# Kernel tuning notes

Measured on AMD Instinct MI355X. Metric: run time of the kernel, lower is better.

The kernel has to match this reference:

```python
import jax, jax.numpy as jnp
import numpy as np

D_MODEL = 1024
NUM_HEADS = 16
D_HEAD = D_MODEL // NUM_HEADS
B, T_Q, T_K = 2, 2048, 2048


def setup_inputs() -> dict:
    key = jax.random.key(0)
    ks = jax.random.split(key, 7)
    s = 0.02
    return {
        "query": jax.random.normal(ks[0], (B, T_Q, D_MODEL), jnp.float32),
        "key_value": jax.random.normal(ks[1], (B, T_K, D_MODEL), jnp.float32),
        "mask": jax.random.randint(ks[2], (B, 1, T_Q, T_K), 0, 2, jnp.int32),
        "rel_pos_bias": jax.random.normal(ks[3], (NUM_HEADS, T_Q, T_K), jnp.float32),
        "Wq": jax.random.normal(ks[4], (D_MODEL, D_MODEL), jnp.float32) * s,
        "Wkv": jax.random.normal(ks[5], (D_MODEL, 2 * D_MODEL), jnp.float32) * s,
        "Wo": jax.random.normal(ks[6], (D_MODEL, D_MODEL), jnp.float32) * s,
    }


def reference(query, key_value, mask, rel_pos_bias, Wq, Wkv, Wo):
    Bq, Tq, D = query.shape
    Tk = key_value.shape[1]
    H, Dh = NUM_HEADS, D_HEAD
    q = (query @ Wq).reshape(Bq, Tq, H, Dh)              # [B,Tq,H,Dh]
    kv = (key_value @ Wkv).reshape(Bq, Tk, 2, H, Dh)
    k, v = kv[:, :, 0], kv[:, :, 1]                      # [B,Tk,H,Dh]
    scale = 1.0 / jnp.sqrt(jnp.asarray(Dh, q.dtype))
    scores = jnp.einsum("bqhd,bkhd->bhqk", q, k) * scale  # [B,H,Tq,Tk]
    scores = scores + rel_pos_bias[None]                  # bias broadcast over batch
    scores = jnp.where(mask == 0, -jnp.inf, scores)
    attn = jax.nn.softmax(scores, axis=-1)
    out = jnp.einsum("bhqk,bkhd->bqhd", attn, v).reshape(Bq, Tq, D)
    return out @ Wo
```

## Files before the change

### kernel.cpp

```cpp
#include <hip/hip_runtime.h>

typedef unsigned short u16;
typedef unsigned int u32;
typedef unsigned long long u64;
typedef __attribute__((ext_vector_type(4))) float f32x4;
typedef __attribute__((ext_vector_type(4))) unsigned short u16x4;
typedef __attribute__((ext_vector_type(8))) short short8;

#define GLOAD16(G, L) __builtin_amdgcn_global_load_lds( \
    (const __attribute__((address_space(1))) void*)(G), \
    (__attribute__((address_space(3))) void*)(L), 16, 0, 0)

__device__ __forceinline__ u16 f2bf(float f) {
  union { float f; unsigned u; } c; c.f = f;
  unsigned u = c.u;
  u += 0x7FFFu + ((u >> 16) & 1u);
  return (u16)(u >> 16);
}

__device__ __forceinline__ void store_out(u16* p, float v) { *p = f2bf(v); }
__device__ __forceinline__ void store_out(float* p, float v) { *p = v; }

__global__ void k_cvt(const float* __restrict__ in, u16* __restrict__ out, int n4) {
  int i = blockIdx.x * blockDim.x + threadIdx.x;
  if (i >= n4) return;
  const f32x4 v = *(const f32x4*)(in + (size_t)i * 4);
  u16x4 o;
  o[0] = f2bf(v[0]); o[1] = f2bf(v[1]); o[2] = f2bf(v[2]); o[3] = f2bf(v[3]);
  *(u16x4*)(out + (size_t)i * 4) = o;
}

__global__ void k_tcvt(const float* __restrict__ src, u16* __restrict__ dst,
                       int R, int C, float scale) {
  __shared__ float t[32][33];
  int bx = blockIdx.x * 32;
  int by = blockIdx.y * 32;
  int tx = threadIdx.x, ty = threadIdx.y;
  #pragma unroll
  for (int j = 0; j < 32; j += 8)
    t[ty + j][tx] = src[(size_t)(by + ty + j) * C + bx + tx];
  __syncthreads();
  #pragma unroll
  for (int j = 0; j < 32; j += 8)
    dst[(size_t)(bx + ty + j) * R + by + tx] = f2bf(t[tx][ty + j] * scale);
}

__global__ void k_tv(const u16* __restrict__ kv, u16* __restrict__ vt) {
  __shared__ u16 sh[32][34];
  int b = blockIdx.z;
  int tb = blockIdx.x * 32;
  int db = blockIdx.y * 32;
  int tx = threadIdx.x, ty = threadIdx.y;
  #pragma unroll
  for (int j = 0; j < 32; j += 8)
    sh[ty + j][tx] = kv[(size_t)(b * 2048 + tb + ty + j) * 2048 + 1024 + db + tx];
  __syncthreads();
  int t = tb + tx;
  int k6 = t & 63;
  int colp = (t & ~63) | (((k6 >> 2) & 3) << 4) | ((k6 >> 4) << 2) | (k6 & 3);
  #pragma unroll
  for (int j = 0; j < 32; j += 8)
    vt[(size_t)(b * 1024 + db + ty + j) * 2048 + colp] = sh[tx][ty + j];
}

__global__ void k_pm(const int* __restrict__ mask, unsigned* __restrict__ bits, int nw) {
  int w = blockIdx.x * blockDim.x + threadIdx.x;
  if (w >= nw) return;
  const int4* p = (const int4*)(mask + (size_t)w * 32);
  unsigned b = 0;
  #pragma unroll
  for (int j = 0; j < 8; ++j) {
    int4 v = p[j];
    b |= (v.x != 0 ? 1u : 0u) << (j * 4);
    b |= (v.y != 0 ? 1u : 0u) << (j * 4 + 1);
    b |= (v.z != 0 ? 1u : 0u) << (j * 4 + 2);
    b |= (v.w != 0 ? 1u : 0u) << (j * 4 + 3);
  }
  bits[w] = b;
}

template <int BM, int BN, typename OUT_T>
__global__ __launch_bounds__(256) void k_gemm(
    const u16* __restrict__ A, const u16* __restrict__ Bt,
    OUT_T* __restrict__ C, int M, int N, int K)
{
  constexpr int MI = BM / 32, NI = BN / 32;
  __shared__ u16 As[BM * 64];
  __shared__ u16 Bs[BN * 64];
  const int tid = threadIdx.x;
  const int lane = tid & 63;
  const int w = tid >> 6;
  const int wr = w >> 1, wc = w & 1;
  const int l16 = lane & 15, lh = lane >> 4;
  const size_t tm = blockIdx.x, tn = blockIdx.y;

  f32x4 acc[MI][NI] = {};

  for (int kt = 0; kt < K; kt += 64) {
    #pragma unroll
    for (int i = 0; i < BM / 32; ++i) {
      int flat = i * 256 + tid;
      int row = flat >> 3, cb = flat & 7;
      GLOAD16(A + (tm * BM + row) * K + kt + ((cb ^ (row & 7)) * 8),
              (char*)As + flat * 16);
    }
    #pragma unroll
    for (int i = 0; i < BN / 32; ++i) {
      int flat = i * 256 + tid;
      int row = flat >> 3, cb = flat & 7;
      GLOAD16(Bt + (tn * BN + row) * K + kt + ((cb ^ (row & 7)) * 8),
              (char*)Bs + flat * 16);
    }
    __syncthreads();
    #pragma unroll
    for (int kk = 0; kk < 2; ++kk) {
      short8 a[MI], b[NI];
      #pragma unroll
      for (int mi = 0; mi < MI; ++mi) {
        int row = wr * (BM / 2) + mi * 16 + l16;
        a[mi] = *(const short8*)&As[row * 64 + ((kk * 32 + lh * 8) ^ ((row & 7) * 8))];
      }
      #pragma unroll
      for (int ni = 0; ni < NI; ++ni) {
        int row = wc * (BN / 2) + ni * 16 + l16;
        b[ni] = *(const short8*)&Bs[row * 64 + ((kk * 32 + lh * 8) ^ ((row & 7) * 8))];
      }
      #pragma unroll
      for (int mi = 0; mi < MI; ++mi)
        #pragma unroll
        for (int ni = 0; ni < NI; ++ni)
          acc[mi][ni] = __builtin_amdgcn_mfma_f32_16x16x32_bf16(a[mi], b[ni], acc[mi][ni], 0, 0, 0);
    }
    __syncthreads();
  }
  #pragma unroll
  for (int mi = 0; mi < MI; ++mi)
    #pragma unroll
    for (int ni = 0; ni < NI; ++ni)
      #pragma unroll
      for (int r = 0; r < 4; ++r) {
        size_t row = tm * BM + wr * (BM / 2) + mi * 16 + lh * 4 + r;
        size_t col = tn * BN + wc * (BN / 2) + ni * 16 + l16;
        store_out(&C[row * N + col], acc[mi][ni][r]);
      }
}

__global__ __launch_bounds__(512, 4) void k_attn(
    const u16* __restrict__ Qp,
    const u16* __restrict__ KVp,
    const u16* __restrict__ Vt,
    const float* __restrict__ bias,
    const unsigned* __restrict__ mbits,
    u16* __restrict__ Ob)
{
  __shared__ u16 Ks[2 * 2 * 64 * 64];
  __shared__ u16 Vs[2 * 2 * 64 * 64];
  const int tid = threadIdx.x;
  const int lane = tid & 63;
  const int w = tid >> 6;
  const int bw = w >> 2;
  const int qs = (w & 3) * 16;
  const int qt = blockIdx.x;
  const int h  = blockIdx.y;
  const int l16 = lane & 15, lh = lane >> 4;
  const int q = qt * 64 + qs + l16;

  const int srow = tid >> 3, scb = tid & 7;
  const u16* ksrc = KVp + (size_t)srow * 2048 + h * 64 + ((scb ^ (srow & 7)) * 8);
  const u16* vsrc = Vt + ((size_t)(h * 64 + srow)) * 2048 + ((scb ^ (srow & 7)) * 8);

  short8 qf[2];
  {
    size_t row = (size_t)bw * 2048 + q;
    qf[0] = *(const short8*)&Qp[row * 1024 + h * 64 + lh * 8];
    qf[1] = *(const short8*)&Qp[row * 1024 + h * 64 + 32 + lh * 8];
  }

  const float* bsrc = bias + ((size_t)h * 2048 + q) * 2048 + lh * 4;
  const u64*   msrc = (const u64*)(mbits + ((size_t)bw * 2048 + q) * 64);

  f32x4 oacc[4] = {};
  f32x4 lpv = {};
  f32x4 biasA[4], biasB[4];
  u64 mwA, mwB;

  GLOAD16(ksrc,                       &Ks[tid * 8]);
  GLOAD16(ksrc + (size_t)2048 * 2048, &Ks[4096 + tid * 8]);
  GLOAD16(vsrc,                       &Vs[tid * 8]);
  GLOAD16(vsrc + (size_t)1024 * 2048, &Vs[4096 + tid * 8]);
  biasA[0] = *(const f32x4*)(bsrc +  0);
  biasA[1] = *(const f32x4*)(bsrc + 16);
  biasA[2] = *(const f32x4*)(bsrc + 32);
  biasA[3] = *(const f32x4*)(bsrc + 48);
  mwA = msrc[0];
  asm volatile("s_waitcnt vmcnt(0)" ::: "memory");
  __builtin_amdgcn_s_barrier();

#define ASTEP(KT, CUR, BC, MC, BN_, MN_) do {                                            \
    const int ktn_ = ((KT) + 1 < 32) ? (KT) + 1 : 31;                                    \
    GLOAD16(ksrc + (size_t)ktn_ * 64 * 2048,                  &Ks[((CUR)^1) * 8192 + tid * 8]);        \
    GLOAD16(ksrc + ((size_t)2048 + (size_t)ktn_ * 64) * 2048, &Ks[((CUR)^1) * 8192 + 4096 + tid * 8]); \
    GLOAD16(vsrc + (size_t)ktn_ * 64,                         &Vs[((CUR)^1) * 8192 + tid * 8]);        \
    GLOAD16(vsrc + (size_t)1024 * 2048 + (size_t)ktn_ * 64,   &Vs[((CUR)^1) * 8192 + 4096 + tid * 8]); \
    __builtin_amdgcn_sched_barrier(0);                                                   \
    f32x4 s_[4];                                                                         \
    s_[0] = BC[0]; s_[1] = BC[1]; s_[2] = BC[2]; s_[3] = BC[3];                          \
    const unsigned tlo_ = (unsigned)(MC) >> (lh * 4);                                    \
    const unsigned thi_ = (unsigned)((MC) >> 32) >> (lh * 4);                            \
    BN_[0] = *(const f32x4*)(bsrc + (size_t)ktn_ * 64 +  0);                             \
    BN_[1] = *(const f32x4*)(bsrc + (size_t)ktn_ * 64 + 16);                             \
    BN_[2] = *(const f32x4*)(bsrc + (size_t)ktn_ * 64 + 32);                             \
    BN_[3] = *(const f32x4*)(bsrc + (size_t)ktn_ * 64 + 48);                             \
    MN_ = msrc[ktn_];                                                                    \
    const int kb_ = (CUR) * 8192 + bw * 4096;                                            \
    _Pragma("unroll")                                                                    \
    for (int kk = 0; kk < 2; ++kk) {                                                     \
      short8 kf_[4];                                                                     \
      _Pragma("unroll")                                                                  \
      for (int ni = 0; ni < 4; ++ni) {                                                   \
        const int row_ = ni * 16 + l16;                                                  \
        kf_[ni] = *(const short8*)&Ks[kb_ + row_ * 64 + ((kk * 32 + lh * 8) ^ ((row_ & 7) * 8))]; \
      }                                                                                  \
      _Pragma("unroll")                                                                  \
      for (int ni = 0; ni < 4; ++ni)                                                     \
        s_[ni] = __builtin_amdgcn_mfma_f32_16x16x32_bf16(kf_[ni], qf[kk], s_[ni], 0, 0, 0); \
    }                                                                                    \
    _Pragma("unroll")                                                                    \
    for (int kk = 0; kk < 2; ++kk) {                                                     \
      union { u32 wd[4]; short8 v; } pf_;                                                \
      _Pragma("unroll")                                                                  \
      for (int half = 0; half < 2; ++half) {                                             \
        const int ni = 2 * kk + half;                                                    \
        const unsigned tw_ = (ni < 2) ? tlo_ : thi_;                                     \
        _Pragma("unroll")                                                                \
        for (int r = 0; r < 4; ++r) {                                                    \
          const unsigned bit_ = (tw_ >> ((ni & 1) * 16 + r)) & 1u;                       \
          float pv_ = bit_ ? __expf(s_[ni][r]) : 0.f;                                    \
          s_[ni][r] = pv_;                                                               \
        }                                                                                \
        lpv += s_[ni];                                                                   \
        asm("v_cvt_pk_bf16_f32 %0, %1, %2" : "=v"(pf_.wd[2*half])   : "v"(s_[ni][0]), "v"(s_[ni][1])); \
        asm("v_cvt_pk_bf16_f32 %0, %1, %2" : "=v"(pf_.wd[2*half+1]) : "v"(s_[ni][2]), "v"(s_[ni][3])); \
      }                                                                                  \
      _Pragma("unroll")                                                                  \
      for (int di = 0; di < 4; ++di) {                                                   \
        const int row_ = di * 16 + l16;                                                  \
        short8 vf_ = *(const short8*)&Vs[kb_ + row_ * 64 + (((lh * 2 + kk) * 8) ^ ((row_ & 7) * 8))]; \
        oacc[di] = __builtin_amdgcn_mfma_f32_16x16x32_bf16(vf_, pf_.v, oacc[di], 0, 0, 0); \
      }                                                                                  \
    }                                                                                    \
    asm volatile("s_waitcnt lgkmcnt(0)" ::: "memory");                                   \
    asm volatile("s_waitcnt vmcnt(5)" ::: "memory");                                     \
    __builtin_amdgcn_s_barrier();                                                        \
  } while (0)

  for (int kt2 = 0; kt2 < 32; kt2 += 2) {
    ASTEP(kt2,     0, biasA, mwA, biasB, mwB);
    ASTEP(kt2 + 1, 1, biasB, mwB, biasA, mwA);
  }
#undef ASTEP

  float lpart = lpv[0] + lpv[1] + lpv[2] + lpv[3];
  lpart += __shfl_xor(lpart, 16);
  lpart += __shfl_xor(lpart, 32);
  float inv = 1.0f / lpart;
  size_t orow = (size_t)bw * 2048 + q;
  #pragma unroll
  for (int di = 0; di < 4; ++di)
    #pragma unroll
    for (int rp = 0; rp < 2; ++rp) {
      float v0 = oacc[di][2 * rp] * inv;
      float v1 = oacc[di][2 * rp + 1] * inv;
      u32 pk;
      asm("v_cvt_pk_bf16_f32 %0, %1, %2" : "=v"(pk) : "v"(v0), "v"(v1));
      *(u32*)&Ob[orow * 1024 + h * 64 + di * 16 + lh * 4 + rp * 2] = pk;
    }
}

extern "C" void kernel_launch(void* const* d_in, const int* in_sizes, int n_in,
                              void* d_out, int out_size, void* d_ws, size_t ws_size,
                              hipStream_t stream) {
  const float* query     = (const float*)d_in[0];
  const float* key_value = (const float*)d_in[1];
  const int*   mask      = (const int*)d_in[2];
  const float* bias      = (const float*)d_in[3];
  const float* Wq        = (const float*)d_in[4];
  const float* Wkv       = (const float*)d_in[5];
  const float* Wo        = (const float*)d_in[6];
  float* out = (float*)d_out;

  char* ws = (char*)d_ws;
  u16* qb   = (u16*)(ws);
  u16* kvb  = (u16*)(ws + 8388608);
  u16* WqT  = (u16*)(ws + 16777216);
  u16* WkvT = (u16*)(ws + 18874368);
  u16* WoT  = (u16*)(ws + 23068672);
  u16* Qp   = (u16*)(ws + 25165824);
  u16* KVp  = (u16*)(ws + 33554432);
  u16* Vt   = (u16*)(ws + 50331648);
  u16* Ob   = (u16*)(ws + 58720256);
  unsigned* mb = (unsigned*)(ws + 67108864);

  dim3 tb(32, 8);
  k_cvt<<<4096, 256, 0, stream>>>(query, qb, 1048576);
  k_cvt<<<4096, 256, 0, stream>>>(key_value, kvb, 1048576);
  k_tcvt<<<dim3(32, 32), tb, 0, stream>>>(Wq,  WqT,  1024, 1024, 0.125f);
  k_tcvt<<<dim3(64, 32), tb, 0, stream>>>(Wkv, WkvT, 1024, 2048, 1.0f);
  k_tcvt<<<dim3(32, 32), tb, 0, stream>>>(Wo,  WoT,  1024, 1024, 1.0f);
  k_pm<<<1024, 256, 0, stream>>>(mask, mb, 262144);
  k_gemm<64, 128, u16><<<dim3(64, 8),  256, 0, stream>>>(qb,  WqT,  Qp,  4096, 1024, 1024);
  k_gemm<64, 128, u16><<<dim3(64, 16), 256, 0, stream>>>(kvb, WkvT, KVp, 4096, 2048, 1024);
  k_tv<<<dim3(64, 32, 2), tb, 0, stream>>>(KVp, Vt);
  k_attn<<<dim3(32, 16), 512, 0, stream>>>(Qp, KVp, Vt, bias, mb, Ob);
  k_gemm<64, 128, float><<<dim3(64, 8), 256, 0, stream>>>(Ob, WoT, out, 4096, 1024, 1024);
}
```

Measured before the change: 223.1 us.

## Process two query sub-tiles per wave in attention to reuse K/V fragments

The attention block drops from 512 to 256 threads, and each wave now handles 32 query rows (two 16-row sub-tiles) instead of 16. Each K and V fragment read from LDS therefore feeds two MFMAs, halving LDS reads per unit of compute, and each thread issues twice as many global-to-LDS copies. s_setprio is raised around the MFMA sections to favour matrix issue. The cost is roughly double the accumulator and bias registers per thread plus fewer waves per block, which may reduce occupancy and latency hiding for the bias and mask loads.

```diff
diff --git a/kernel.cpp b/kernel.cpp
--- a/kernel.cpp
+++ b/kernel.cpp
@@ -145,7 +145,7 @@
       }
 }
 
-__global__ __launch_bounds__(512, 4) void k_attn(
+__global__ __launch_bounds__(256, 2) void k_attn(
     const u16* __restrict__ Qp,
     const u16* __restrict__ KVp,
     const u16* __restrict__ Vt,
@@ -158,61 +158,87 @@
   const int tid = threadIdx.x;
   const int lane = tid & 63;
   const int w = tid >> 6;
-  const int bw = w >> 2;
-  const int qs = (w & 3) * 16;
+  const int bw = w >> 1;
+  const int qs = (w & 1) * 32;
   const int qt = blockIdx.x;
   const int h  = blockIdx.y;
   const int l16 = lane & 15, lh = lane >> 4;
-  const int q = qt * 64 + qs + l16;
-
-  const int srow = tid >> 3, scb = tid & 7;
-  const u16* ksrc = KVp + (size_t)srow * 2048 + h * 64 + ((scb ^ (srow & 7)) * 8);
-  const u16* vsrc = Vt + ((size_t)(h * 64 + srow)) * 2048 + ((scb ^ (srow & 7)) * 8);
-
-  short8 qf[2];
+  const int q0 = qt * 64 + qs + l16;
+
+  const int sr0 = tid >> 3;
+  const int sc0 = (((tid & 7)) ^ (sr0 & 7)) * 8;
+  const int sr1 = (256 + tid) >> 3;
+  const int sc1 = ((((256 + tid) & 7)) ^ (sr1 & 7)) * 8;
+  const u16* k0 = KVp + (size_t)sr0 * 2048 + h * 64 + sc0;
+  const u16* k1 = KVp + (size_t)sr1 * 2048 + h * 64 + sc1;
+  const u16* v0 = Vt + (size_t)(h * 64 + sr0) * 2048 + sc0;
+  const u16* v1 = Vt + (size_t)(h * 64 + sr1) * 2048 + sc1;
+
+  short8 qf0[2], qf1[2];
   {
-    size_t row = (size_t)bw * 2048 + q;
-    qf[0] = *(const short8*)&Qp[row * 1024 + h * 64 + lh * 8];
-    qf[1] = *(const short8*)&Qp[row * 1024 + h * 64 + 32 + lh * 8];
-  }
-
-  const float* bsrc = bias + ((size_t)h * 2048 + q) * 2048 + lh * 4;
-  const u64*   msrc = (const u64*)(mbits + ((size_t)bw * 2048 + q) * 64);
-
-  f32x4 oacc[4] = {};
-  f32x4 lpv = {};
-  f32x4 biasA[4], biasB[4];
-  u64 mwA, mwB;
-
-  GLOAD16(ksrc,                       &Ks[tid * 8]);
-  GLOAD16(ksrc + (size_t)2048 * 2048, &Ks[4096 + tid * 8]);
-  GLOAD16(vsrc,                       &Vs[tid * 8]);
-  GLOAD16(vsrc + (size_t)1024 * 2048, &Vs[4096 + tid * 8]);
-  biasA[0] = *(const f32x4*)(bsrc +  0);
-  biasA[1] = *(const f32x4*)(bsrc + 16);
-  biasA[2] = *(const f32x4*)(bsrc + 32);
-  biasA[3] = *(const f32x4*)(bsrc + 48);
-  mwA = msrc[0];
+    size_t row = (size_t)bw * 2048 + q0;
+    qf0[0] = *(const short8*)&Qp[row * 1024 + h * 64 + lh * 8];
+    qf0[1] = *(const short8*)&Qp[row * 1024 + h * 64 + 32 + lh * 8];
+    qf1[0] = *(const short8*)&Qp[(row + 16) * 1024 + h * 64 + lh * 8];
+    qf1[1] = *(const short8*)&Qp[(row + 16) * 1024 + h * 64 + 32 + lh * 8];
+  }
+
+  const float* bsrc0 = bias + ((size_t)h * 2048 + q0) * 2048 + lh * 4;
+  const float* bsrc1 = bsrc0 + (size_t)16 * 2048;
+  const u64* msrc0 = (const u64*)(mbits + ((size_t)bw * 2048 + q0) * 64);
+  const u64* msrc1 = msrc0 + 16 * 32;
+
+  f32x4 oacc0[4] = {}, oacc1[4] = {};
+  f32x4 lpv0 = {}, lpv1 = {};
+  f32x4 bA0[4], bA1[4], bB0[4], bB1[4];
+  u64 mA0, mA1, mB0, mB1;
+
+  GLOAD16(k0,                       &Ks[tid * 8]);
+  GLOAD16(k1,                       &Ks[2048 + tid * 8]);
+  GLOAD16(k0 + (size_t)2048 * 2048, &Ks[4096 + tid * 8]);
+  GLOAD16(k1 + (size_t)2048 * 2048, &Ks[6144 + tid * 8]);
+  GLOAD16(v0,                       &Vs[tid * 8]);
+  GLOAD16(v1,                       &Vs[2048 + tid * 8]);
+  GLOAD16(v0 + (size_t)1024 * 2048, &Vs[4096 + tid * 8]);
+  GLOAD16(v1 + (size_t)1024 * 2048, &Vs[6144 + tid * 8]);
+  #pragma unroll
+  for (int ni = 0; ni < 4; ++ni) {
+    bA0[ni] = *(const f32x4*)(bsrc0 + ni * 16);
+    bA1[ni] = *(const f32x4*)(bsrc1 + ni * 16);
+  }
+  mA0 = msrc0[0];
+  mA1 = msrc1[0];
   asm volatile("s_waitcnt vmcnt(0)" ::: "memory");
   __builtin_amdgcn_s_barrier();
 
-#define ASTEP(KT, CUR, BC, MC, BN_, MN_) do {                                            \
+#define ASTEP(KT, CUR, BC0, BC1, MC0, MC1, BN0, BN1, MN0, MN1) do {                      \
     const int ktn_ = ((KT) + 1 < 32) ? (KT) + 1 : 31;                                    \
-    GLOAD16(ksrc + (size_t)ktn_ * 64 * 2048,                  &Ks[((CUR)^1) * 8192 + tid * 8]);        \
-    GLOAD16(ksrc + ((size_t)2048 + (size_t)ktn_ * 64) * 2048, &Ks[((CUR)^1) * 8192 + 4096 + tid * 8]); \
-    GLOAD16(vsrc + (size_t)ktn_ * 64,                         &Vs[((CUR)^1) * 8192 + tid * 8]);        \
-    GLOAD16(vsrc + (size_t)1024 * 2048 + (size_t)ktn_ * 64,   &Vs[((CUR)^1) * 8192 + 4096 + tid * 8]); \
+    const int nb_ = (CUR) ^ 1;                                                           \
+    GLOAD16(k0 + (size_t)ktn_ * 64 * 2048,                  &Ks[nb_ * 8192 + tid * 8]);  \
+    GLOAD16(k1 + (size_t)ktn_ * 64 * 2048,                  &Ks[nb_ * 8192 + 2048 + tid * 8]); \
+    GLOAD16(k0 + ((size_t)2048 + ktn_ * 64) * 2048,         &Ks[nb_ * 8192 + 4096 + tid * 8]); \
+    GLOAD16(k1 + ((size_t)2048 + ktn_ * 64) * 2048,         &Ks[nb_ * 8192 + 6144 + tid * 8]); \
+    GLOAD16(v0 + (size_t)ktn_ * 64,                         &Vs[nb_ * 8192 + tid * 8]);  \
+    GLOAD16(v1 + (size_t)ktn_ * 64,                         &Vs[nb_ * 8192 + 2048 + tid * 8]); \
+    GLOAD16(v0 + (size_t)1024 * 2048 + ktn_ * 64,           &Vs[nb_ * 8192 + 4096 + tid * 8]); \
+    GLOAD16(v1 + (size_t)1024 * 2048 + ktn_ * 64,           &Vs[nb_ * 8192 + 6144 + tid * 8]); \
     __builtin_amdgcn_sched_barrier(0);                                                   \
-    f32x4 s_[4];                                                                         \
-    s_[0] = BC[0]; s_[1] = BC[1]; s_[2] = BC[2]; s_[3] = BC[3];                          \
-    const unsigned tlo_ = (unsigned)(MC) >> (lh * 4);                                    \
-    const unsigned thi_ = (unsigned)((MC) >> 32) >> (lh * 4);                            \
-    BN_[0] = *(const f32x4*)(bsrc + (size_t)ktn_ * 64 +  0);                             \
-    BN_[1] = *(const f32x4*)(bsrc + (size_t)ktn_ * 64 + 16);                             \
-    BN_[2] = *(const f32x4*)(bsrc + (size_t)ktn_ * 64 + 32);                             \
-    BN_[3] = *(const f32x4*)(bsrc + (size_t)ktn_ * 64 + 48);                             \
-    MN_ = msrc[ktn_];                                                                    \
+    f32x4 s0_[4], s1_[4];                                                                \
+    _Pragma("unroll")                                                                    \
+    for (int ni = 0; ni < 4; ++ni) { s0_[ni] = BC0[ni]; s1_[ni] = BC1[ni]; }             \
+    const unsigned tlo0_ = (unsigned)(MC0) >> (lh * 4);                                  \
+    const unsigned thi0_ = (unsigned)((MC0) >> 32) >> (lh * 4);                          \
+    const unsigned tlo1_ = (unsigned)(MC1) >> (lh * 4);                                  \
+    const unsigned thi1_ = (unsigned)((MC1) >> 32) >> (lh * 4);                          \
+    _Pragma("unroll")                                                                    \
+    for (int ni = 0; ni < 4; ++ni) {                                                     \
+      BN0[ni] = *(const f32x4*)(bsrc0 + (size_t)ktn_ * 64 + ni * 16);                    \
+      BN1[ni] = *(const f32x4*)(bsrc1 + (size_t)ktn_ * 64 + ni * 16);                    \
+    }                                                                                    \
+    MN0 = msrc0[ktn_];                                                                   \
+    MN1 = msrc1[ktn_];                                                                   \
     const int kb_ = (CUR) * 8192 + bw * 4096;                                            \
+    __builtin_amdgcn_s_setprio(1);                                                       \
     _Pragma("unroll")                                                                    \
     for (int kk = 0; kk < 2; ++kk) {                                                     \
       short8 kf_[4];                                                                     \
@@ -222,59 +248,89 @@
         kf_[ni] = *(const short8*)&Ks[kb_ + row_ * 64 + ((kk * 32 + lh * 8) ^ ((row_ & 7) * 8))]; \
       }                                                                                  \
       _Pragma("unroll")                                                                  \
-      for (int ni = 0; ni < 4; ++ni)                                                     \
-        s_[ni] = __builtin_amdgcn_mfma_f32_16x16x32_bf16(kf_[ni], qf[kk], s_[ni], 0, 0, 0); \
+      for (int ni = 0; ni < 4; ++ni) {                                                   \
+        s0_[ni] = __builtin_amdgcn_mfma_f32_16x16x32_bf16(kf_[ni], qf0[kk], s0_[ni], 0, 0, 0); \
+        s1_[ni] = __builtin_amdgcn_mfma_f32_16x16x32_bf16(kf_[ni], qf1[kk], s1_[ni], 0, 0, 0); \
+      }                                                                                  \
     }                                                                                    \
+    __builtin_amdgcn_s_setprio(0);                                                       \
+    union pfu_ { u32 wd[4]; short8 v; };                                                 \
+    union pfu_ pf0_[2], pf1_[2];                                                         \
+    _Pragma("unroll")                                                                    \
+    for (int ni = 0; ni < 4; ++ni) {                                                     \
+      const unsigned tw0_ = (ni < 2) ? tlo0_ : thi0_;                                    \
+      const unsigned tw1_ = (ni < 2) ? tlo1_ : thi1_;                                    \
+      _Pragma("unroll")                                                                  \
+      for (int r = 0; r < 4; ++r) {                                                      \
+        const unsigned b0_ = (tw0_ >> ((ni & 1) * 16 + r)) & 1u;                         \
+        const unsigned b1_ = (tw1_ >> ((ni & 1) * 16 + r)) & 1u;                         \
+        s0_[ni][r] = b0_ ? __expf(s0_[ni][r]) : 0.f;                                     \
+        s1_[ni][r] = b1_ ? __expf(s1_[ni][r]) : 0.f;                                     \
+      }                                                                                  \
+      lpv0 += s0_[ni];                                                                   \
+      lpv1 += s1_[ni];                                                                   \
+      asm("v_cvt_pk_bf16_f32 %0, %1, %2" : "=v"(pf0_[ni >> 1].wd[2 * (ni & 1)])     : "v"(s0_[ni][0]), "v"(s0_[ni][1])); \
+      asm("v_cvt_pk_bf16_f32 %0, %1, %2" : "=v"(pf0_[ni >> 1].wd[2 * (ni & 1) + 1]) : "v"(s0_[ni][2]), "v"(s0_[ni][3])); \
+      asm("v_cvt_pk_bf16_f32 %0, %1, %2" : "=v"(pf1_[ni >> 1].wd[2 * (ni & 1)])     : "v"(s1_[ni][0]), "v"(s1_[ni][1])); \
+      asm("v_cvt_pk_bf16_f32 %0, %1, %2" : "=v"(pf1_[ni >> 1].wd[2 * (ni & 1) + 1]) : "v"(s1_[ni][2]), "v"(s1_[ni][3])); \
+    }                                                                                    \
+    __builtin_amdgcn_s_setprio(1);                                                       \
     _Pragma("unroll")                                                                    \
     for (int kk = 0; kk < 2; ++kk) {                                                     \
-      union { u32 wd[4]; short8 v; } pf_;                                                \
-      _Pragma("unroll")                                                                  \
-      for (int half = 0; half < 2; ++half) {                                             \
-        const int ni = 2 * kk + half;                                                    \
-        const unsigned tw_ = (ni < 2) ? tlo_ : thi_;                                     \
-        _Pragma("unroll")                                                                \
-        for (int r = 0; r < 4; ++r) {                                                    \
-          const unsigned bit_ = (tw_ >> ((ni & 1) * 16 + r)) & 1u;                       \
-          float pv_ = bit_ ? __expf(s_[ni][r]) : 0.f;                                    \
-          s_[ni][r] = pv_;                                                               \
-        }                                                                                \
-        lpv += s_[ni];                                                                   \
-        asm("v_cvt_pk_bf16_f32 %0, %1, %2" : "=v"(pf_.wd[2*half])   : "v"(s_[ni][0]), "v"(s_[ni][1])); \
-        asm("v_cvt_pk_bf16_f32 %0, %1, %2" : "=v"(pf_.wd[2*half+1]) : "v"(s_[ni][2]), "v"(s_[ni][3])); \
-      }                                                                                  \
       _Pragma("unroll")                                                                  \
       for (int di = 0; di < 4; ++di) {                                                   \
         const int row_ = di * 16 + l16;                                                  \
         short8 vf_ = *(const short8*)&Vs[kb_ + row_ * 64 + (((lh * 2 + kk) * 8) ^ ((row_ & 7) * 8))]; \
-        oacc[di] = __builtin_amdgcn_mfma_f32_16x16x32_bf16(vf_, pf_.v, oacc[di], 0, 0, 0); \
+        oacc0[di] = __builtin_amdgcn_mfma_f32_16x16x32_bf16(vf_, pf0_[kk].v, oacc0[di], 0, 0, 0); \
+        oacc1[di] = __builtin_amdgcn_mfma_f32_16x16x32_bf16(vf_, pf1_[kk].v, oacc1[di], 0, 0, 0); \
       }                                                                                  \
     }                                                                                    \
+    __builtin_amdgcn_s_setprio(0);                                                       \
     asm volatile("s_waitcnt lgkmcnt(0)" ::: "memory");                                   \
-    asm volatile("s_waitcnt vmcnt(5)" ::: "memory");                                     \
+    asm volatile("s_waitcnt vmcnt(10)" ::: "memory");                                    \
     __builtin_amdgcn_s_barrier();                                                        \
   } while (0)
 
   for (int kt2 = 0; kt2 < 32; kt2 += 2) {
-    ASTEP(kt2,     0, biasA, mwA, biasB, mwB);
-    ASTEP(kt2 + 1, 1, biasB, mwB, biasA, mwA);
+    ASTEP(kt2,     0, bA0, bA1, mA0, mA1, bB0, bB1, mB0, mB1);
+    ASTEP(kt2 + 1, 1, bB0, bB1, mB0, mB1, bA0, bA1, mA0, mA1);
   }
 #undef ASTEP
 
-  float lpart = lpv[0] + lpv[1] + lpv[2] + lpv[3];
-  lpart += __shfl_xor(lpart, 16);
-  lpart += __shfl_xor(lpart, 32);
-  float inv = 1.0f / lpart;
-  size_t orow = (size_t)bw * 2048 + q;
-  #pragma unroll
-  for (int di = 0; di < 4; ++di)
-    #pragma unroll
-    for (int rp = 0; rp < 2; ++rp) {
-      float v0 = oacc[di][2 * rp] * inv;
-      float v1 = oacc[di][2 * rp + 1] * inv;
-      u32 pk;
-      asm("v_cvt_pk_bf16_f32 %0, %1, %2" : "=v"(pk) : "v"(v0), "v"(v1));
-      *(u32*)&Ob[orow * 1024 + h * 64 + di * 16 + lh * 4 + rp * 2] = pk;
-    }
+  {
+    float lp = lpv0[0] + lpv0[1] + lpv0[2] + lpv0[3];
+    lp += __shfl_xor(lp, 16);
+    lp += __shfl_xor(lp, 32);
+    float inv = 1.0f / lp;
+    size_t orow = (size_t)bw * 2048 + q0;
+    #pragma unroll
+    for (int di = 0; di < 4; ++di)
+      #pragma unroll
+      for (int rp = 0; rp < 2; ++rp) {
+        float a = oacc0[di][2 * rp] * inv;
+        float b = oacc0[di][2 * rp + 1] * inv;
+        u32 pk;
+        asm("v_cvt_pk_bf16_f32 %0, %1, %2" : "=v"(pk) : "v"(a), "v"(b));
+        *(u32*)&Ob[orow * 1024 + h * 64 + di * 16 + lh * 4 + rp * 2] = pk;
+      }
+  }
+  {
+    float lp = lpv1[0] + lpv1[1] + lpv1[2] + lpv1[3];
+    lp += __shfl_xor(lp, 16);
+    lp += __shfl_xor(lp, 32);
+    float inv = 1.0f / lp;
+    size_t orow = (size_t)bw * 2048 + q0 + 16;
+    #pragma unroll
+    for (int di = 0; di < 4; ++di)
+      #pragma unroll
+      for (int rp = 0; rp < 2; ++rp) {
+        float a = oacc1[di][2 * rp] * inv;
+        float b = oacc1[di][2 * rp + 1] * inv;
+        u32 pk;
+        asm("v_cvt_pk_bf16_f32 %0, %1, %2" : "=v"(pk) : "v"(a), "v"(b));
+        *(u32*)&Ob[orow * 1024 + h * 64 + di * 16 + lh * 4 + rp * 2] = pk;
+      }
+  }
 }
 
 extern "C" void kernel_launch(void* const* d_in, const int* in_sizes, int n_in,
@@ -311,6 +367,6 @@
   k_gemm<64, 128, u16><<<dim3(64, 8),  256, 0, stream>>>(qb,  WqT,  Qp,  4096, 1024, 1024);
   k_gemm<64, 128, u16><<<dim3(64, 16), 256, 0, stream>>>(kvb, WkvT, KVp, 4096, 2048, 1024);
   k_tv<<<dim3(64, 32, 2), tb, 0, stream>>>(KVp, Vt);
-  k_attn<<<dim3(32, 16), 512, 0, stream>>>(Qp, KVp, Vt, bias, mb, Ob);
+  k_attn<<<dim3(32, 16), 256, 0, stream>>>(Qp, KVp, Vt, bias, mb, Ob);
   k_gemm<64, 128, float><<<dim3(64, 8), 256, 0, stream>>>(Ob, WoT, out, 4096, 1024, 1024);
 }
```

Result: slower. 228.3 us (+2.3%).

## Load V fragments directly from global, shrink attention blocks, swizzle block order

Applied to the files above, without the earlier changes.

Reworks the attention kernel. Blocks shrink to 256 threads covering 32 queries, and the grid doubles. The V tile is no longer staged in LDS: each wave reads its V fragments straight from global memory (the transposed Vt buffer) into registers, which frees LDS and barrier traffic. It also remaps block IDs so blocks sharing a head land near each other, adds s_setprio around the MFMA sections, and relaxes the vmcnt wait. The risk is extra global-load latency and less K reuse per block, since K tiles are now loaded by twice as many blocks.

```diff
diff --git a/kernel.cpp b/kernel.cpp
--- a/kernel.cpp
+++ b/kernel.cpp
@@ -145,7 +145,7 @@
       }
 }
 
-__global__ __launch_bounds__(512, 4) void k_attn(
+__global__ __launch_bounds__(256, 3) void k_attn(
     const u16* __restrict__ Qp,
     const u16* __restrict__ KVp,
     const u16* __restrict__ Vt,
@@ -154,20 +154,22 @@
     u16* __restrict__ Ob)
 {
   __shared__ u16 Ks[2 * 2 * 64 * 64];
-  __shared__ u16 Vs[2 * 2 * 64 * 64];
   const int tid = threadIdx.x;
   const int lane = tid & 63;
   const int w = tid >> 6;
-  const int bw = w >> 2;
-  const int qs = (w & 3) * 16;
-  const int qt = blockIdx.x;
-  const int h  = blockIdx.y;
+  const int bw = w >> 1;
+  const int qg = w & 1;
+  const int bid = blockIdx.y * 64 + blockIdx.x;
+  const int sid = (bid & 7) * 128 + (bid >> 3);
+  const int qt = sid & 63;
+  const int h  = sid >> 6;
   const int l16 = lane & 15, lh = lane >> 4;
-  const int q = qt * 64 + qs + l16;
-
-  const int srow = tid >> 3, scb = tid & 7;
-  const u16* ksrc = KVp + (size_t)srow * 2048 + h * 64 + ((scb ^ (srow & 7)) * 8);
-  const u16* vsrc = Vt + ((size_t)(h * 64 + srow)) * 2048 + ((scb ^ (srow & 7)) * 8);
+  const int q = qt * 32 + qg * 16 + l16;
+
+  const int r0 = tid >> 3, cb = tid & 7;
+  const u16* kbase0 = KVp + (size_t)r0 * 2048 + h * 64 + ((cb ^ (r0 & 7)) * 8);
+
+  const u16* vptr = Vt + ((size_t)(bw * 1024 + h * 64 + l16)) * 2048 + lh * 16;
 
   short8 qf[2];
   {
@@ -182,26 +184,27 @@
   f32x4 oacc[4] = {};
   f32x4 lpv = {};
   f32x4 biasA[4], biasB[4];
-  u64 mwA, mwB;
-
-  GLOAD16(ksrc,                       &Ks[tid * 8]);
-  GLOAD16(ksrc + (size_t)2048 * 2048, &Ks[4096 + tid * 8]);
-  GLOAD16(vsrc,                       &Vs[tid * 8]);
-  GLOAD16(vsrc + (size_t)1024 * 2048, &Vs[4096 + tid * 8]);
-  biasA[0] = *(const f32x4*)(bsrc +  0);
-  biasA[1] = *(const f32x4*)(bsrc + 16);
-  biasA[2] = *(const f32x4*)(bsrc + 32);
-  biasA[3] = *(const f32x4*)(bsrc + 48);
-  mwA = msrc[0];
+  u64 mA, mB;
+
+  GLOAD16(kbase0,                            &Ks[tid * 8]);
+  GLOAD16(kbase0 + 65536,                    &Ks[2048 + tid * 8]);
+  GLOAD16(kbase0 + (size_t)2048 * 2048,      &Ks[4096 + tid * 8]);
+  GLOAD16(kbase0 + (size_t)2048 * 2048 + 65536, &Ks[6144 + tid * 8]);
+  #pragma unroll
+  for (int ni = 0; ni < 4; ++ni)
+    biasA[ni] = *(const f32x4*)(bsrc + ni * 16);
+  mA = msrc[0];
   asm volatile("s_waitcnt vmcnt(0)" ::: "memory");
   __builtin_amdgcn_s_barrier();
 
 #define ASTEP(KT, CUR, BC, MC, BN_, MN_) do {                                            \
     const int ktn_ = ((KT) + 1 < 32) ? (KT) + 1 : 31;                                    \
-    GLOAD16(ksrc + (size_t)ktn_ * 64 * 2048,                  &Ks[((CUR)^1) * 8192 + tid * 8]);        \
-    GLOAD16(ksrc + ((size_t)2048 + (size_t)ktn_ * 64) * 2048, &Ks[((CUR)^1) * 8192 + 4096 + tid * 8]); \
-    GLOAD16(vsrc + (size_t)ktn_ * 64,                         &Vs[((CUR)^1) * 8192 + tid * 8]);        \
-    GLOAD16(vsrc + (size_t)1024 * 2048 + (size_t)ktn_ * 64,   &Vs[((CUR)^1) * 8192 + 4096 + tid * 8]); \
+    const int nb_ = (CUR) ^ 1;                                                           \
+    const size_t kro_ = (size_t)ktn_ * 64 * 2048;                                        \
+    GLOAD16(kbase0 + kro_,                               &Ks[nb_ * 8192 + tid * 8]);     \
+    GLOAD16(kbase0 + kro_ + 65536,                       &Ks[nb_ * 8192 + 2048 + tid * 8]); \
+    GLOAD16(kbase0 + kro_ + (size_t)2048 * 2048,         &Ks[nb_ * 8192 + 4096 + tid * 8]); \
+    GLOAD16(kbase0 + kro_ + (size_t)2048 * 2048 + 65536, &Ks[nb_ * 8192 + 6144 + tid * 8]); \
     __builtin_amdgcn_sched_barrier(0);                                                   \
     f32x4 s_[4];                                                                         \
     s_[0] = BC[0]; s_[1] = BC[1]; s_[2] = BC[2]; s_[3] = BC[3];                          \
@@ -213,6 +216,7 @@
     BN_[3] = *(const f32x4*)(bsrc + (size_t)ktn_ * 64 + 48);                             \
     MN_ = msrc[ktn_];                                                                    \
     const int kb_ = (CUR) * 8192 + bw * 4096;                                            \
+    __builtin_amdgcn_s_setprio(1);                                                       \
     _Pragma("unroll")                                                                    \
     for (int kk = 0; kk < 2; ++kk) {                                                     \
       short8 kf_[4];                                                                     \
@@ -225,38 +229,41 @@
       for (int ni = 0; ni < 4; ++ni)                                                     \
         s_[ni] = __builtin_amdgcn_mfma_f32_16x16x32_bf16(kf_[ni], qf[kk], s_[ni], 0, 0, 0); \
     }                                                                                    \
+    __builtin_amdgcn_s_setprio(0);                                                       \
+    short8 vf_[4][2];                                                                    \
     _Pragma("unroll")                                                                    \
-    for (int kk = 0; kk < 2; ++kk) {                                                     \
-      union { u32 wd[4]; short8 v; } pf_;                                                \
+    for (int di = 0; di < 4; ++di) {                                                     \
+      vf_[di][0] = *(const short8*)(vptr + (size_t)di * 16 * 2048 + (size_t)(KT) * 64);      \
+      vf_[di][1] = *(const short8*)(vptr + (size_t)di * 16 * 2048 + (size_t)(KT) * 64 + 8);  \
+    }                                                                                    \
+    union pfu_ { u32 wd[4]; short8 v; };                                                 \
+    union pfu_ pf_[2];                                                                   \
+    _Pragma("unroll")                                                                    \
+    for (int ni = 0; ni < 4; ++ni) {                                                     \
+      const unsigned tw_ = (ni < 2) ? tlo_ : thi_;                                       \
       _Pragma("unroll")                                                                  \
-      for (int half = 0; half < 2; ++half) {                                             \
-        const int ni = 2 * kk + half;                                                    \
-        const unsigned tw_ = (ni < 2) ? tlo_ : thi_;                                     \
-        _Pragma("unroll")                                                                \
-        for (int r = 0; r < 4; ++r) {                                                    \
-          const unsigned bit_ = (tw_ >> ((ni & 1) * 16 + r)) & 1u;                       \
-          float pv_ = bit_ ? __expf(s_[ni][r]) : 0.f;                                    \
-          s_[ni][r] = pv_;                                                               \
-        }                                                                                \
-        lpv += s_[ni];                                                                   \
-        asm("v_cvt_pk_bf16_f32 %0, %1, %2" : "=v"(pf_.wd[2*half])   : "v"(s_[ni][0]), "v"(s_[ni][1])); \
-        asm("v_cvt_pk_bf16_f32 %0, %1, %2" : "=v"(pf_.wd[2*half+1]) : "v"(s_[ni][2]), "v"(s_[ni][3])); \
+      for (int r = 0; r < 4; ++r) {                                                      \
+        const unsigned bit_ = (tw_ >> ((ni & 1) * 16 + r)) & 1u;                         \
+        s_[ni][r] = bit_ ? __expf(s_[ni][r]) : 0.f;                                      \
       }                                                                                  \
+      lpv += s_[ni];                                                                     \
+      asm("v_cvt_pk_bf16_f32 %0, %1, %2" : "=v"(pf_[ni >> 1].wd[2 * (ni & 1)])     : "v"(s_[ni][0]), "v"(s_[ni][1])); \
+      asm("v_cvt_pk_bf16_f32 %0, %1, %2" : "=v"(pf_[ni >> 1].wd[2 * (ni & 1) + 1]) : "v"(s_[ni][2]), "v"(s_[ni][3])); \
+    }                                                                                    \
+    __builtin_amdgcn_s_setprio(1);                                                       \
+    _Pragma("unroll")                                                                    \
+    for (int kk = 0; kk < 2; ++kk)                                                       \
       _Pragma("unroll")                                                                  \
-      for (int di = 0; di < 4; ++di) {                                                   \
-        const int row_ = di * 16 + l16;                                                  \
-        short8 vf_ = *(const short8*)&Vs[kb_ + row_ * 64 + (((lh * 2 + kk) * 8) ^ ((row_ & 7) * 8))]; \
-        oacc[di] = __builtin_amdgcn_mfma_f32_16x16x32_bf16(vf_, pf_.v, oacc[di], 0, 0, 0); \
-      }                                                                                  \
-    }                                                                                    \
-    asm volatile("s_waitcnt lgkmcnt(0)" ::: "memory");                                   \
-    asm volatile("s_waitcnt vmcnt(5)" ::: "memory");                                     \
+      for (int di = 0; di < 4; ++di)                                                     \
+        oacc[di] = __builtin_amdgcn_mfma_f32_16x16x32_bf16(vf_[di][kk], pf_[kk].v, oacc[di], 0, 0, 0); \
+    __builtin_amdgcn_s_setprio(0);                                                       \
+    asm volatile("s_waitcnt vmcnt(13)" ::: "memory");                                    \
     __builtin_amdgcn_s_barrier();                                                        \
   } while (0)
 
   for (int kt2 = 0; kt2 < 32; kt2 += 2) {
-    ASTEP(kt2,     0, biasA, mwA, biasB, mwB);
-    ASTEP(kt2 + 1, 1, biasB, mwB, biasA, mwA);
+    ASTEP(kt2,     0, biasA, mA, biasB, mB);
+    ASTEP(kt2 + 1, 1, biasB, mB, biasA, mA);
   }
 #undef ASTEP
 
@@ -311,6 +318,6 @@
   k_gemm<64, 128, u16><<<dim3(64, 8),  256, 0, stream>>>(qb,  WqT,  Qp,  4096, 1024, 1024);
   k_gemm<64, 128, u16><<<dim3(64, 16), 256, 0, stream>>>(kvb, WkvT, KVp, 4096, 2048, 1024);
   k_tv<<<dim3(64, 32, 2), tb, 0, stream>>>(KVp, Vt);
-  k_attn<<<dim3(32, 16), 512, 0, stream>>>(Qp, KVp, Vt, bias, mb, Ob);
+  k_attn<<<dim3(64, 16), 256, 0, stream>>>(Qp, KVp, Vt, bias, mb, Ob);
   k_gemm<64, 128, float><<<dim3(64, 8), 256, 0, stream>>>(Ob, WoT, out, 4096, 1024, 1024);
 }
```

Result: slower. 330.9 us (+48.3%).
